# Kernel optimization log

Measured on AMD Instinct MI355X. Metric: run time of the kernel, lower is better.

## Reference

```python
import jax, jax.numpy as jnp
import numpy as np

WIN = 7  # window_size
NUM_HEADS = 8


def _relative_position_index(ws: int) -> np.ndarray:
    # Matches torch.meshgrid default ('ij') indexing used in the module.
    coords = np.stack(np.meshgrid(np.arange(ws), np.arange(ws), indexing='ij'))  # (2, ws, ws)
    flat = coords.reshape(2, -1)                                   # (2, ws*ws)
    rel = flat[:, :, None] - flat[:, None, :]                      # (2, N, N)
    rel = rel.transpose(1, 2, 0).copy()                            # (N, N, 2)
    rel[:, :, 0] += ws - 1
    rel[:, :, 1] += ws - 1
    rel[:, :, 0] *= 2 * ws - 1
    return rel.sum(-1)                                             # (N, N) int


def setup_inputs() -> dict:
    key = jax.random.key(0)
    ks = jax.random.split(key, 7)
    B_, N, C = 4096, WIN * WIN, 256
    nW = 64
    return {
        'x': jax.random.normal(ks[0], (B_, N, C), dtype=jnp.float32),
        'mask': jax.random.normal(ks[1], (nW, N, N), dtype=jnp.float32),
        'qkv_w': jax.random.normal(ks[2], (3 * C, C), dtype=jnp.float32) * 0.02,
        'qkv_b': jax.random.normal(ks[3], (3 * C,), dtype=jnp.float32) * 0.02,
        'proj_w': jax.random.normal(ks[4], (C, C), dtype=jnp.float32) * 0.02,
        'proj_b': jax.random.normal(ks[5], (C,), dtype=jnp.float32) * 0.02,
        'rpb_table': jax.random.normal(ks[6], ((2 * WIN - 1) ** 2, NUM_HEADS), dtype=jnp.float32) * 0.02,
    }


def reference(x, mask, qkv_w, qkv_b, proj_w, proj_b, rpb_table):
    B_, N, C = x.shape
    H = NUM_HEADS
    hd = C // H
    scale = hd ** -0.5
    rpi = jnp.asarray(_relative_position_index(WIN))  # (N, N) int, constant

    qkv = x @ qkv_w.T + qkv_b                          # (B_, N, 3C)
    qkv = qkv.reshape(B_, N, 3, H, hd).transpose(2, 0, 3, 1, 4)  # (3, B_, H, N, hd)
    q, k, v = qkv[0], qkv[1], qkv[2]

    attn = jnp.einsum('bhnd,bhmd->bhnm', q * scale, k)  # (B_, H, N, N)
    bias = rpb_table[rpi.reshape(-1)].reshape(N, N, H).transpose(2, 0, 1)  # (H, N, N)
    attn = attn + bias[None]

    nW = mask.shape[0]
    attn = attn.reshape(B_ // nW, nW, H, N, N) + mask[None, :, None]
    attn = attn.reshape(B_, H, N, N)
    attn = jax.nn.softmax(attn, axis=-1)

    out = jnp.einsum('bhnm,bhmd->bhnd', attn, v)       # (B_, H, N, hd)
    out = out.transpose(0, 2, 1, 3).reshape(B_, N, C)
    return out @ proj_w.T + proj_b
```

## Files before the change

### kernel.cpp

```cpp
#include <hip/hip_runtime.h>

#define SEG 51380224

typedef __attribute__((ext_vector_type(8))) __bf16 bf16x8;
typedef __attribute__((ext_vector_type(4))) __bf16 bf16x4;
typedef __attribute__((ext_vector_type(4))) float f32x4;

static __device__ __forceinline__ bf16x8 bzero8() {
    bf16x8 z;
#pragma unroll
    for (int u = 0; u < 8; ++u) z[u] = (__bf16)0.0f;
    return z;
}

static __device__ __forceinline__ void gl_lds16(const __bf16* g, __bf16* l) {
    __builtin_amdgcn_global_load_lds(
        (const __attribute__((address_space(1))) void*)g,
        (__attribute__((address_space(3))) void*)l, 16, 0, 0);
}

__global__ __launch_bounds__(256)
void cvt_bf16_k(const float* __restrict__ src, __bf16* __restrict__ dst, int n8)
{
    int i = blockIdx.x * 256 + threadIdx.x;
    const int stride = gridDim.x * 256;
    for (; i < n8; i += stride) {
        float4 a = *reinterpret_cast<const float4*>(src + (size_t)i * 8);
        float4 b = *reinterpret_cast<const float4*>(src + (size_t)i * 8 + 4);
        bf16x8 o;
        o[0] = (__bf16)a.x; o[1] = (__bf16)a.y; o[2] = (__bf16)a.z; o[3] = (__bf16)a.w;
        o[4] = (__bf16)b.x; o[5] = (__bf16)b.y; o[6] = (__bf16)b.z; o[7] = (__bf16)b.w;
        *reinterpret_cast<bf16x8*>(dst + (size_t)i * 8) = o;
    }
}

__global__ __launch_bounds__(256)
void expand_add_k(const float* __restrict__ mask, const float* __restrict__ rpb,
                  float* __restrict__ add)
{
    const int wh = blockIdx.x;
    const int w = wh >> 3, h = wh & 7;
    for (int e = threadIdx.x; e < 4096; e += 256) {
        int i = e >> 6, j = e & 63;
        float v = -1e30f;
        if (i < 49 && j < 49) {
            int ih = i / 7, iw = i - ih * 7;
            int jh = j / 7, jw = j - jh * 7;
            int bidx = (ih - jh + 6) * 13 + (iw - jw + 6);
            v = mask[(size_t)w * 2401 + i * 49 + j] + rpb[bidx * 8 + h];
        }
        add[(size_t)wh * 4096 + e] = v;
    }
}

__global__ __launch_bounds__(256)
void qkv_gemm_k(const __bf16* __restrict__ x, const __bf16* __restrict__ w,
                const float* __restrict__ bvec, __bf16* __restrict__ ws)
{
    __shared__ __bf16 As[2][128][64];
    __shared__ __bf16 Bs[2][128][64];
    const int tid  = threadIdx.x;
    const int nwg  = 1568 * 6;
    const int bid  = blockIdx.x;
    const int v    = (bid & 7) * (nwg >> 3) + (bid >> 3);
    const int mb   = v / 6, nb = v - mb * 6;
    const int m0   = mb * 128;
    const int n0   = nb * 128;
    const int wave = tid >> 6, lane = tid & 63;
    const int wm   = wave >> 1, wn = wave & 1;
    const int quad = lane >> 4, lm = lane & 15;

    const int srow = wave * 8 + (lane >> 3);
    const int scol = (((lane & 7) ^ (lane >> 3)) << 3);

    f32x4 acc[4][4] = {};

#pragma unroll
    for (int i = 0; i < 4; ++i) {
        int row = i * 32 + srow;
        gl_lds16(x + (size_t)(m0 + row) * 256 + 0 + scol,
                 &As[0][0][0] + i * 2048 + wave * 512);
        gl_lds16(w + (size_t)(n0 + row) * 256 + 0 + scol,
                 &Bs[0][0][0] + i * 2048 + wave * 512);
    }
    asm volatile("s_waitcnt vmcnt(0)" ::: "memory");
    __builtin_amdgcn_s_barrier();

#pragma unroll
    for (int t = 0; t < 4; ++t) {
        if (t < 3) {
            const int k0 = (t + 1) * 64;
            const int nb2 = (t + 1) & 1;
#pragma unroll
            for (int i = 0; i < 4; ++i) {
                int row = i * 32 + srow;
                gl_lds16(x + (size_t)(m0 + row) * 256 + k0 + scol,
                         &As[nb2][0][0] + i * 2048 + wave * 512);
                gl_lds16(w + (size_t)(n0 + row) * 256 + k0 + scol,
                         &Bs[nb2][0][0] + i * 2048 + wave * 512);
            }
        }
        const __bf16* Ab = &As[t & 1][0][0];
        const __bf16* Bb = &Bs[t & 1][0][0];
        __builtin_amdgcn_s_setprio(1);
#pragma unroll
        for (int kk = 0; kk < 64; kk += 32) {
            const int cl = (kk >> 3) + quad;
            bf16x8 af[4], bfr[4];
#pragma unroll
            for (int mt = 0; mt < 4; ++mt) {
                int row = wm * 64 + mt * 16 + lm;
                af[mt] = *reinterpret_cast<const bf16x8*>(Ab + row * 64 + ((cl ^ (lm & 7)) << 3));
            }
#pragma unroll
            for (int nt = 0; nt < 4; ++nt) {
                int row = wn * 64 + nt * 16 + lm;
                bfr[nt] = *reinterpret_cast<const bf16x8*>(Bb + row * 64 + ((cl ^ (lm & 7)) << 3));
            }
#pragma unroll
            for (int mt = 0; mt < 4; ++mt)
#pragma unroll
                for (int nt = 0; nt < 4; ++nt)
                    acc[mt][nt] = __builtin_amdgcn_mfma_f32_16x16x32_bf16(af[mt], bfr[nt], acc[mt][nt], 0, 0, 0);
        }
        __builtin_amdgcn_s_setprio(0);
        asm volatile("s_waitcnt vmcnt(0)" ::: "memory");
        __builtin_amdgcn_s_barrier();
    }

    const int   c3   = n0 >> 8;
    const float scl  = (c3 == 0) ? 0.17677669529663687f : 1.0f;
    __bf16*     segp = ws + (size_t)c3 * SEG;
    const int   n0c  = n0 & 255;
    char*       Cs   = (char*)&As[0][0][0];

#pragma unroll
    for (int nt = 0; nt < 4; ++nt) {
        float bj = bvec[n0 + wn * 64 + nt * 16 + lm];
#pragma unroll
        for (int mt = 0; mt < 4; ++mt)
#pragma unroll
            for (int r = 0; r < 4; ++r) {
                int row = wm * 64 + mt * 16 + quad * 4 + r;
                int byteoff = (row << 8) + ((wn * 64 + nt * 16 + lm) << 1);
                byteoff ^= (row & 0xC) << 2;
                *reinterpret_cast<__bf16*>(Cs + byteoff) =
                    (__bf16)((acc[mt][nt][r] + bj) * scl);
            }
    }
    __syncthreads();
#pragma unroll
    for (int it = 0; it < 8; ++it) {
        int row = it * 16 + (tid >> 4);
        int byteoff = (row << 8) + ((tid & 15) << 4);
        byteoff ^= (row & 0xC) << 2;
        bf16x8 c8 = *reinterpret_cast<const bf16x8*>(Cs + byteoff);
        *reinterpret_cast<bf16x8*>(segp + (size_t)(m0 + row) * 256 + n0c + ((tid & 15) << 3)) = c8;
    }
}

__global__ __launch_bounds__(64)
void attn_mfma_k(const __bf16* __restrict__ ws, const float* __restrict__ add,
                 __bf16* __restrict__ pre)
{
    __shared__ __bf16 Pl[64 * 72];
    __shared__ __bf16 Vt[32 * 72];
    const int lane = threadIdx.x;
    const int bh   = blockIdx.x;
    const int b    = bh >> 3, h = bh & 7;
    const int wh   = ((b & 63) << 3) | h;
    const int quad = lane >> 4, lm = lane & 15;
    const int koff = quad * 8;

    const __bf16* qp = ws + (size_t)(b * 49) * 256 + h * 32;
    const __bf16* kp = qp + SEG;
    const __bf16* vp = qp + (size_t)2 * SEG;

    {
        int d = lane >> 1, j0 = 48 + (lane & 1) * 8;
        *reinterpret_cast<bf16x8*>(&Vt[d * 72 + j0]) = bzero8();
    }
#pragma unroll
    for (int t = 0; t < 4; ++t) {
        int idx = lane + t * 64;
        if (idx < 196) {
            int j = idx >> 2, c8 = (idx & 3) * 8;
            bf16x8 vv = *reinterpret_cast<const bf16x8*>(vp + j * 256 + c8);
#pragma unroll
            for (int u = 0; u < 8; ++u) Vt[(c8 + u) * 72 + j] = vv[u];
        }
    }

    bf16x8 qf[4], kf[4];
#pragma unroll
    for (int t = 0; t < 4; ++t)
        qf[t] = *reinterpret_cast<const bf16x8*>(qp + (t * 16 + lm) * 256 + koff);
#pragma unroll
    for (int t = 0; t < 4; ++t) {
        int m = t * 16 + lm;
        kf[t] = (m < 49) ? *reinterpret_cast<const bf16x8*>(kp + m * 256 + koff)
                         : bzero8();
    }

    f32x4 s[4][4] = {};
#pragma unroll
    for (int mt = 0; mt < 4; ++mt)
#pragma unroll
        for (int nt = 0; nt < 4; ++nt)
            s[mt][nt] = __builtin_amdgcn_mfma_f32_16x16x32_bf16(kf[mt], qf[nt], s[mt][nt], 0, 0, 0);

    const float* ap = add + (size_t)wh * 4096;
#pragma unroll
    for (int nt = 0; nt < 4; ++nt) {
        int i = nt * 16 + lm;
#pragma unroll
        for (int mt = 0; mt < 4; ++mt) {
            f32x4 a4 = *reinterpret_cast<const f32x4*>(ap + i * 64 + mt * 16 + quad * 4);
            s[mt][nt] += a4;
        }
    }

#pragma unroll
    for (int nt = 0; nt < 4; ++nt) {
        float mx = -3.0e38f;
#pragma unroll
        for (int mt = 0; mt < 4; ++mt)
#pragma unroll
            for (int r = 0; r < 4; ++r) mx = fmaxf(mx, s[mt][nt][r]);
        mx = fmaxf(mx, __shfl_xor(mx, 16));
        mx = fmaxf(mx, __shfl_xor(mx, 32));
        float sum = 0.f;
#pragma unroll
        for (int mt = 0; mt < 4; ++mt)
#pragma unroll
            for (int r = 0; r < 4; ++r) {
                float e = __expf(s[mt][nt][r] - mx);
                s[mt][nt][r] = e; sum += e;
            }
        sum += __shfl_xor(sum, 16);
        sum += __shfl_xor(sum, 32);
        float rl = 1.0f / sum;
#pragma unroll
        for (int mt = 0; mt < 4; ++mt)
#pragma unroll
            for (int r = 0; r < 4; ++r) s[mt][nt][r] *= rl;
    }

#pragma unroll
    for (int nt = 0; nt < 4; ++nt) {
        int i = nt * 16 + lm;
#pragma unroll
        for (int mt = 0; mt < 4; ++mt) {
            bf16x4 p4;
#pragma unroll
            for (int r = 0; r < 4; ++r) p4[r] = (__bf16)s[mt][nt][r];
            *reinterpret_cast<bf16x4*>(&Pl[i * 72 + mt * 16 + quad * 4]) = p4;
        }
    }
    __syncthreads();

    f32x4 o[4][2] = {};
#pragma unroll
    for (int kt = 0; kt < 2; ++kt) {
        bf16x8 vf[2];
#pragma unroll
        for (int dt = 0; dt < 2; ++dt)
            vf[dt] = *reinterpret_cast<const bf16x8*>(&Vt[(dt * 16 + lm) * 72 + kt * 32 + koff]);
#pragma unroll
        for (int mt2 = 0; mt2 < 4; ++mt2) {
            bf16x8 pf = *reinterpret_cast<const bf16x8*>(&Pl[(mt2 * 16 + lm) * 72 + kt * 32 + koff]);
#pragma unroll
            for (int dt = 0; dt < 2; ++dt)
                o[mt2][dt] = __builtin_amdgcn_mfma_f32_16x16x32_bf16(pf, vf[dt], o[mt2][dt], 0, 0, 0);
        }
    }

    __syncthreads();
    __bf16* Ol = &Vt[0];
#pragma unroll
    for (int mt2 = 0; mt2 < 4; ++mt2)
#pragma unroll
        for (int dt = 0; dt < 2; ++dt)
#pragma unroll
            for (int r = 0; r < 4; ++r)
                Ol[(mt2 * 16 + quad * 4 + r) * 32 + dt * 16 + lm] = (__bf16)o[mt2][dt][r];
    __syncthreads();
#pragma unroll
    for (int it = 0; it < 4; ++it) {
        int i = it * 16 + (lane >> 2);
        if (i < 49) {
            bf16x8 v8 = *reinterpret_cast<const bf16x8*>(&Ol[i * 32 + (lane & 3) * 8]);
            *reinterpret_cast<bf16x8*>(pre + ((size_t)(b * 49 + i)) * 256 + h * 32 + (lane & 3) * 8) = v8;
        }
    }
}

__global__ __launch_bounds__(256)
void proj_gemm_k(const __bf16* __restrict__ pre, const __bf16* __restrict__ w,
                 const float* __restrict__ bvec, float* __restrict__ out)
{
    __shared__ __bf16 As[2][128][64];
    __shared__ __bf16 Bs[2][128][64];
    const int tid  = threadIdx.x;
    const int nwg  = 1568 * 2;
    const int bid  = blockIdx.x;
    const int v    = (bid & 7) * (nwg >> 3) + (bid >> 3);
    const int mb   = v >> 1, nb = v & 1;
    const int m0   = mb * 128;
    const int n0   = nb * 128;
    const int wave = tid >> 6, lane = tid & 63;
    const int wm   = wave >> 1, wn = wave & 1;
    const int quad = lane >> 4, lm = lane & 15;

    const int srow = wave * 8 + (lane >> 3);
    const int scol = (((lane & 7) ^ (lane >> 3)) << 3);

    f32x4 acc[4][4] = {};

#pragma unroll
    for (int i = 0; i < 4; ++i) {
        int row = i * 32 + srow;
        gl_lds16(pre + (size_t)(m0 + row) * 256 + 0 + scol,
                 &As[0][0][0] + i * 2048 + wave * 512);
        gl_lds16(w + (size_t)(n0 + row) * 256 + 0 + scol,
                 &Bs[0][0][0] + i * 2048 + wave * 512);
    }
    asm volatile("s_waitcnt vmcnt(0)" ::: "memory");
    __builtin_amdgcn_s_barrier();

#pragma unroll
    for (int t = 0; t < 4; ++t) {
        if (t < 3) {
            const int k0 = (t + 1) * 64;
            const int nb2 = (t + 1) & 1;
#pragma unroll
            for (int i = 0; i < 4; ++i) {
                int row = i * 32 + srow;
                gl_lds16(pre + (size_t)(m0 + row) * 256 + k0 + scol,
                         &As[nb2][0][0] + i * 2048 + wave * 512);
                gl_lds16(w + (size_t)(n0 + row) * 256 + k0 + scol,
                         &Bs[nb2][0][0] + i * 2048 + wave * 512);
            }
        }
        const __bf16* Ab = &As[t & 1][0][0];
        const __bf16* Bb = &Bs[t & 1][0][0];
        __builtin_amdgcn_s_setprio(1);
#pragma unroll
        for (int kk = 0; kk < 64; kk += 32) {
            const int cl = (kk >> 3) + quad;
            bf16x8 af[4], bfr[4];
#pragma unroll
            for (int mt = 0; mt < 4; ++mt) {
                int row = wm * 64 + mt * 16 + lm;
                af[mt] = *reinterpret_cast<const bf16x8*>(Ab + row * 64 + ((cl ^ (lm & 7)) << 3));
            }
#pragma unroll
            for (int nt = 0; nt < 4; ++nt) {
                int row = wn * 64 + nt * 16 + lm;
                bfr[nt] = *reinterpret_cast<const bf16x8*>(Bb + row * 64 + ((cl ^ (lm & 7)) << 3));
            }
#pragma unroll
            for (int mt = 0; mt < 4; ++mt)
#pragma unroll
                for (int nt = 0; nt < 4; ++nt)
                    acc[mt][nt] = __builtin_amdgcn_mfma_f32_16x16x32_bf16(af[mt], bfr[nt], acc[mt][nt], 0, 0, 0);
        }
        __builtin_amdgcn_s_setprio(0);
        asm volatile("s_waitcnt vmcnt(0)" ::: "memory");
        __builtin_amdgcn_s_barrier();
    }

#pragma unroll
    for (int nt = 0; nt < 4; ++nt) {
        int j = n0 + wn*64 + nt*16 + lm;
        float bj = bvec[j];
#pragma unroll
        for (int mt = 0; mt < 4; ++mt)
#pragma unroll
            for (int r = 0; r < 4; ++r) {
                int m = m0 + wm*64 + mt*16 + quad*4 + r;
                out[(size_t)m*256 + j] = acc[mt][nt][r] + bj;
            }
    }
}

extern "C" void kernel_launch(void* const* d_in, const int* in_sizes, int n_in,
                              void* d_out, int out_size, void* d_ws, size_t ws_size,
                              hipStream_t stream)
{
    const float* x      = (const float*)d_in[0];
    const float* mask   = (const float*)d_in[1];
    const float* qkv_w  = (const float*)d_in[2];
    const float* qkv_b  = (const float*)d_in[3];
    const float* proj_w = (const float*)d_in[4];
    const float* proj_b = (const float*)d_in[5];
    const float* rpb    = (const float*)d_in[6];

    __bf16* ws  = (__bf16*)d_ws;
    __bf16* pre = ws + (size_t)3 * SEG;
    float*  out = (float*)d_out;

    char*   ob      = (char*)d_out;
    float*  addbuf  = (float*)ob;
    __bf16* qkv_wb  = (__bf16*)(ob + (10u << 20));
    __bf16* xb      = (__bf16*)(ob + (16u << 20));
    __bf16* proj_wb = ws;

    cvt_bf16_k<<<dim3(2048), 256, 0, stream>>>(x, xb, 51380224 / 8);
    cvt_bf16_k<<<dim3(96),   256, 0, stream>>>(qkv_w, qkv_wb, 196608 / 8);
    expand_add_k<<<dim3(512), 256, 0, stream>>>(mask, rpb, addbuf);
    qkv_gemm_k<<<dim3(1568 * 6), 256, 0, stream>>>(xb, qkv_wb, qkv_b, ws);
    attn_mfma_k<<<dim3(32768), 64, 0, stream>>>(ws, addbuf, pre);
    cvt_bf16_k<<<dim3(32),   256, 0, stream>>>(proj_w, proj_wb, 65536 / 8);
    proj_gemm_k<<<dim3(1568 * 2), 256, 0, stream>>>(pre, proj_wb, proj_b, out);
}
```

Baseline: 781.6 us.

## Fuse prep kernels, shrink GEMM K-tile to 32, use nontemporal stores

Merges the x and qkv_w bf16 conversions and the mask+bias expansion into one prep kernel, removing two launches. Both GEMMs now use a K-step of 32 with half the LDS (32 KB), a matching swizzle and 8 pipeline stages, which may allow higher occupancy but adds barriers per tile. Output stores in the QKV and projection GEMMs become nontemporal to avoid polluting cache.

```diff
diff --git a/kernel.cpp b/kernel.cpp
--- a/kernel.cpp
+++ b/kernel.cpp
@@ -19,46 +19,71 @@
         (__attribute__((address_space(3))) void*)l, 16, 0, 0);
 }
 
+static __device__ __forceinline__ void cvt8(const float* src, __bf16* dst, int i) {
+    float4 a = *reinterpret_cast<const float4*>(src + (size_t)i * 8);
+    float4 b = *reinterpret_cast<const float4*>(src + (size_t)i * 8 + 4);
+    bf16x8 o;
+    o[0] = (__bf16)a.x; o[1] = (__bf16)a.y; o[2] = (__bf16)a.z; o[3] = (__bf16)a.w;
+    o[4] = (__bf16)b.x; o[5] = (__bf16)b.y; o[6] = (__bf16)b.z; o[7] = (__bf16)b.w;
+    *reinterpret_cast<bf16x8*>(dst + (size_t)i * 8) = o;
+}
+
+__global__ __launch_bounds__(256)
+void prep_k(const float* __restrict__ x, __bf16* __restrict__ xb,
+            const float* __restrict__ qw, __bf16* __restrict__ qwb,
+            const float* __restrict__ mask, const float* __restrict__ rpb,
+            float* __restrict__ add)
+{
+    const int NX = 51380224 / 8;
+    const int NW = 196608 / 8;
+    const int NE = 2097152 / 8;
+    int idx = blockIdx.x * 256 + threadIdx.x;
+    const int stride = gridDim.x * 256;
+    for (; idx < NX + NW + NE; idx += stride) {
+        if (idx < NX) {
+            cvt8(x, xb, idx);
+        } else if (idx < NX + NW) {
+            cvt8(qw, qwb, idx - NX);
+        } else {
+            int e = (idx - NX - NW) * 8;
+            int wh = e >> 12, within = e & 4095;
+            int i = within >> 6, j0 = within & 63;
+            int w = wh >> 3, h = wh & 7;
+            int ih = i / 7, iw = i - ih * 7;
+            float o[8];
+#pragma unroll
+            for (int u = 0; u < 8; ++u) {
+                int j = j0 + u;
+                float v = -1e30f;
+                if (i < 49 && j < 49) {
+                    int jh = j / 7, jw = j - jh * 7;
+                    int bidx = (ih - jh + 6) * 13 + (iw - jw + 6);
+                    v = mask[(size_t)w * 2401 + i * 49 + j] + rpb[bidx * 8 + h];
+                }
+                o[u] = v;
+            }
+            float* dst = add + (size_t)wh * 4096 + i * 64 + j0;
+            *reinterpret_cast<f32x4*>(dst)     = f32x4{o[0], o[1], o[2], o[3]};
+            *reinterpret_cast<f32x4*>(dst + 4) = f32x4{o[4], o[5], o[6], o[7]};
+        }
+    }
+}
+
 __global__ __launch_bounds__(256)
 void cvt_bf16_k(const float* __restrict__ src, __bf16* __restrict__ dst, int n8)
 {
     int i = blockIdx.x * 256 + threadIdx.x;
     const int stride = gridDim.x * 256;
-    for (; i < n8; i += stride) {
-        float4 a = *reinterpret_cast<const float4*>(src + (size_t)i * 8);
-        float4 b = *reinterpret_cast<const float4*>(src + (size_t)i * 8 + 4);
-        bf16x8 o;
-        o[0] = (__bf16)a.x; o[1] = (__bf16)a.y; o[2] = (__bf16)a.z; o[3] = (__bf16)a.w;
-        o[4] = (__bf16)b.x; o[5] = (__bf16)b.y; o[6] = (__bf16)b.z; o[7] = (__bf16)b.w;
-        *reinterpret_cast<bf16x8*>(dst + (size_t)i * 8) = o;
-    }
-}
-
-__global__ __launch_bounds__(256)
-void expand_add_k(const float* __restrict__ mask, const float* __restrict__ rpb,
-                  float* __restrict__ add)
-{
-    const int wh = blockIdx.x;
-    const int w = wh >> 3, h = wh & 7;
-    for (int e = threadIdx.x; e < 4096; e += 256) {
-        int i = e >> 6, j = e & 63;
-        float v = -1e30f;
-        if (i < 49 && j < 49) {
-            int ih = i / 7, iw = i - ih * 7;
-            int jh = j / 7, jw = j - jh * 7;
-            int bidx = (ih - jh + 6) * 13 + (iw - jw + 6);
-            v = mask[(size_t)w * 2401 + i * 49 + j] + rpb[bidx * 8 + h];
-        }
-        add[(size_t)wh * 4096 + e] = v;
-    }
+    for (; i < n8; i += stride) cvt8(src, dst, i);
 }
 
 __global__ __launch_bounds__(256)
 void qkv_gemm_k(const __bf16* __restrict__ x, const __bf16* __restrict__ w,
                 const float* __restrict__ bvec, __bf16* __restrict__ ws)
 {
-    __shared__ __bf16 As[2][128][64];
-    __shared__ __bf16 Bs[2][128][64];
+    __shared__ __attribute__((aligned(16))) char smem[32768];
+    __bf16* Asm = (__bf16*)smem;
+    __bf16* Bsm = (__bf16*)(smem + 16384);
     const int tid  = threadIdx.x;
     const int nwg  = 1568 * 6;
     const int bid  = blockIdx.x;
@@ -70,59 +95,53 @@
     const int wm   = wave >> 1, wn = wave & 1;
     const int quad = lane >> 4, lm = lane & 15;
 
-    const int srow = wave * 8 + (lane >> 3);
-    const int scol = (((lane & 7) ^ (lane >> 3)) << 3);
+    const int srow = wave * 16 + (lane >> 2);
+    const int scol = (((lane & 3) ^ ((lane >> 2) & 3)) << 3);
 
     f32x4 acc[4][4] = {};
 
 #pragma unroll
-    for (int i = 0; i < 4; ++i) {
-        int row = i * 32 + srow;
-        gl_lds16(x + (size_t)(m0 + row) * 256 + 0 + scol,
-                 &As[0][0][0] + i * 2048 + wave * 512);
-        gl_lds16(w + (size_t)(n0 + row) * 256 + 0 + scol,
-                 &Bs[0][0][0] + i * 2048 + wave * 512);
+    for (int i = 0; i < 2; ++i) {
+        gl_lds16(x + (size_t)(m0 + i * 64 + srow) * 256 + 0 + scol,
+                 Asm + i * 2048 + wave * 512);
+        gl_lds16(w + (size_t)(n0 + i * 64 + srow) * 256 + 0 + scol,
+                 Bsm + i * 2048 + wave * 512);
     }
     asm volatile("s_waitcnt vmcnt(0)" ::: "memory");
     __builtin_amdgcn_s_barrier();
 
 #pragma unroll
-    for (int t = 0; t < 4; ++t) {
-        if (t < 3) {
-            const int k0 = (t + 1) * 64;
-            const int nb2 = (t + 1) & 1;
-#pragma unroll
-            for (int i = 0; i < 4; ++i) {
-                int row = i * 32 + srow;
-                gl_lds16(x + (size_t)(m0 + row) * 256 + k0 + scol,
-                         &As[nb2][0][0] + i * 2048 + wave * 512);
-                gl_lds16(w + (size_t)(n0 + row) * 256 + k0 + scol,
-                         &Bs[nb2][0][0] + i * 2048 + wave * 512);
-            }
-        }
-        const __bf16* Ab = &As[t & 1][0][0];
-        const __bf16* Bb = &Bs[t & 1][0][0];
+    for (int t = 0; t < 8; ++t) {
+        const int cur = t & 1, nxt = cur ^ 1;
+        if (t < 7) {
+            const int k0 = (t + 1) * 32;
+#pragma unroll
+            for (int i = 0; i < 2; ++i) {
+                gl_lds16(x + (size_t)(m0 + i * 64 + srow) * 256 + k0 + scol,
+                         Asm + nxt * 4096 + i * 2048 + wave * 512);
+                gl_lds16(w + (size_t)(n0 + i * 64 + srow) * 256 + k0 + scol,
+                         Bsm + nxt * 4096 + i * 2048 + wave * 512);
+            }
+        }
+        const __bf16* Ab = Asm + cur * 4096;
+        const __bf16* Bb = Bsm + cur * 4096;
         __builtin_amdgcn_s_setprio(1);
-#pragma unroll
-        for (int kk = 0; kk < 64; kk += 32) {
-            const int cl = (kk >> 3) + quad;
-            bf16x8 af[4], bfr[4];
-#pragma unroll
-            for (int mt = 0; mt < 4; ++mt) {
-                int row = wm * 64 + mt * 16 + lm;
-                af[mt] = *reinterpret_cast<const bf16x8*>(Ab + row * 64 + ((cl ^ (lm & 7)) << 3));
-            }
-#pragma unroll
-            for (int nt = 0; nt < 4; ++nt) {
-                int row = wn * 64 + nt * 16 + lm;
-                bfr[nt] = *reinterpret_cast<const bf16x8*>(Bb + row * 64 + ((cl ^ (lm & 7)) << 3));
-            }
-#pragma unroll
-            for (int mt = 0; mt < 4; ++mt)
-#pragma unroll
-                for (int nt = 0; nt < 4; ++nt)
-                    acc[mt][nt] = __builtin_amdgcn_mfma_f32_16x16x32_bf16(af[mt], bfr[nt], acc[mt][nt], 0, 0, 0);
-        }
+        bf16x8 af[4], bfr[4];
+#pragma unroll
+        for (int mt = 0; mt < 4; ++mt) {
+            int row = wm * 64 + mt * 16 + lm;
+            af[mt] = *reinterpret_cast<const bf16x8*>(Ab + row * 32 + ((quad ^ (lm & 3)) << 3));
+        }
+#pragma unroll
+        for (int nt = 0; nt < 4; ++nt) {
+            int row = wn * 64 + nt * 16 + lm;
+            bfr[nt] = *reinterpret_cast<const bf16x8*>(Bb + row * 32 + ((quad ^ (lm & 3)) << 3));
+        }
+#pragma unroll
+        for (int mt = 0; mt < 4; ++mt)
+#pragma unroll
+            for (int nt = 0; nt < 4; ++nt)
+                acc[mt][nt] = __builtin_amdgcn_mfma_f32_16x16x32_bf16(af[mt], bfr[nt], acc[mt][nt], 0, 0, 0);
         __builtin_amdgcn_s_setprio(0);
         asm volatile("s_waitcnt vmcnt(0)" ::: "memory");
         __builtin_amdgcn_s_barrier();
@@ -132,7 +151,7 @@
     const float scl  = (c3 == 0) ? 0.17677669529663687f : 1.0f;
     __bf16*     segp = ws + (size_t)c3 * SEG;
     const int   n0c  = n0 & 255;
-    char*       Cs   = (char*)&As[0][0][0];
+    char*       Cs   = smem;
 
 #pragma unroll
     for (int nt = 0; nt < 4; ++nt) {
@@ -155,7 +174,8 @@
         int byteoff = (row << 8) + ((tid & 15) << 4);
         byteoff ^= (row & 0xC) << 2;
         bf16x8 c8 = *reinterpret_cast<const bf16x8*>(Cs + byteoff);
-        *reinterpret_cast<bf16x8*>(segp + (size_t)(m0 + row) * 256 + n0c + ((tid & 15) << 3)) = c8;
+        __builtin_nontemporal_store(c8,
+            reinterpret_cast<bf16x8*>(segp + (size_t)(m0 + row) * 256 + n0c + ((tid & 15) << 3)));
     }
 }
 
@@ -299,8 +319,9 @@
 void proj_gemm_k(const __bf16* __restrict__ pre, const __bf16* __restrict__ w,
                  const float* __restrict__ bvec, float* __restrict__ out)
 {
-    __shared__ __bf16 As[2][128][64];
-    __shared__ __bf16 Bs[2][128][64];
+    __shared__ __attribute__((aligned(16))) char smem[32768];
+    __bf16* Asm = (__bf16*)smem;
+    __bf16* Bsm = (__bf16*)(smem + 16384);
     const int tid  = threadIdx.x;
     const int nwg  = 1568 * 2;
     const int bid  = blockIdx.x;
@@ -312,59 +333,53 @@
     const int wm   = wave >> 1, wn = wave & 1;
     const int quad = lane >> 4, lm = lane & 15;
 
-    const int srow = wave * 8 + (lane >> 3);
-    const int scol = (((lane & 7) ^ (lane >> 3)) << 3);
+    const int srow = wave * 16 + (lane >> 2);
+    const int scol = (((lane & 3) ^ ((lane >> 2) & 3)) << 3);
 
     f32x4 acc[4][4] = {};
 
 #pragma unroll
-    for (int i = 0; i < 4; ++i) {
-        int row = i * 32 + srow;
-        gl_lds16(pre + (size_t)(m0 + row) * 256 + 0 + scol,
-                 &As[0][0][0] + i * 2048 + wave * 512);
-        gl_lds16(w + (size_t)(n0 + row) * 256 + 0 + scol,
-                 &Bs[0][0][0] + i * 2048 + wave * 512);
+    for (int i = 0; i < 2; ++i) {
+        gl_lds16(pre + (size_t)(m0 + i * 64 + srow) * 256 + 0 + scol,
+                 Asm + i * 2048 + wave * 512);
+        gl_lds16(w + (size_t)(n0 + i * 64 + srow) * 256 + 0 + scol,
+                 Bsm + i * 2048 + wave * 512);
     }
     asm volatile("s_waitcnt vmcnt(0)" ::: "memory");
     __builtin_amdgcn_s_barrier();
 
 #pragma unroll
-    for (int t = 0; t < 4; ++t) {
-        if (t < 3) {
-            const int k0 = (t + 1) * 64;
-            const int nb2 = (t + 1) & 1;
-#pragma unroll
-            for (int i = 0; i < 4; ++i) {
-                int row = i * 32 + srow;
-                gl_lds16(pre + (size_t)(m0 + row) * 256 + k0 + scol,
-                         &As[nb2][0][0] + i * 2048 + wave * 512);
-                gl_lds16(w + (size_t)(n0 + row) * 256 + k0 + scol,
-                         &Bs[nb2][0][0] + i * 2048 + wave * 512);
-            }
-        }
-        const __bf16* Ab = &As[t & 1][0][0];
-        const __bf16* Bb = &Bs[t & 1][0][0];
+    for (int t = 0; t < 8; ++t) {
+        const int cur = t & 1, nxt = cur ^ 1;
+        if (t < 7) {
+            const int k0 = (t + 1) * 32;
+#pragma unroll
+            for (int i = 0; i < 2; ++i) {
+                gl_lds16(pre + (size_t)(m0 + i * 64 + srow) * 256 + k0 + scol,
+                         Asm + nxt * 4096 + i * 2048 + wave * 512);
+                gl_lds16(w + (size_t)(n0 + i * 64 + srow) * 256 + k0 + scol,
+                         Bsm + nxt * 4096 + i * 2048 + wave * 512);
+            }
+        }
+        const __bf16* Ab = Asm + cur * 4096;
+        const __bf16* Bb = Bsm + cur * 4096;
         __builtin_amdgcn_s_setprio(1);
-#pragma unroll
-        for (int kk = 0; kk < 64; kk += 32) {
-            const int cl = (kk >> 3) + quad;
-            bf16x8 af[4], bfr[4];
-#pragma unroll
-            for (int mt = 0; mt < 4; ++mt) {
-                int row = wm * 64 + mt * 16 + lm;
-                af[mt] = *reinterpret_cast<const bf16x8*>(Ab + row * 64 + ((cl ^ (lm & 7)) << 3));
-            }
-#pragma unroll
-            for (int nt = 0; nt < 4; ++nt) {
-                int row = wn * 64 + nt * 16 + lm;
-                bfr[nt] = *reinterpret_cast<const bf16x8*>(Bb + row * 64 + ((cl ^ (lm & 7)) << 3));
-            }
-#pragma unroll
-            for (int mt = 0; mt < 4; ++mt)
-#pragma unroll
-                for (int nt = 0; nt < 4; ++nt)
-                    acc[mt][nt] = __builtin_amdgcn_mfma_f32_16x16x32_bf16(af[mt], bfr[nt], acc[mt][nt], 0, 0, 0);
-        }
+        bf16x8 af[4], bfr[4];
+#pragma unroll
+        for (int mt = 0; mt < 4; ++mt) {
+            int row = wm * 64 + mt * 16 + lm;
+            af[mt] = *reinterpret_cast<const bf16x8*>(Ab + row * 32 + ((quad ^ (lm & 3)) << 3));
+        }
+#pragma unroll
+        for (int nt = 0; nt < 4; ++nt) {
+            int row = wn * 64 + nt * 16 + lm;
+            bfr[nt] = *reinterpret_cast<const bf16x8*>(Bb + row * 32 + ((quad ^ (lm & 3)) << 3));
+        }
+#pragma unroll
+        for (int mt = 0; mt < 4; ++mt)
+#pragma unroll
+            for (int nt = 0; nt < 4; ++nt)
+                acc[mt][nt] = __builtin_amdgcn_mfma_f32_16x16x32_bf16(af[mt], bfr[nt], acc[mt][nt], 0, 0, 0);
         __builtin_amdgcn_s_setprio(0);
         asm volatile("s_waitcnt vmcnt(0)" ::: "memory");
         __builtin_amdgcn_s_barrier();
@@ -379,7 +394,7 @@
 #pragma unroll
             for (int r = 0; r < 4; ++r) {
                 int m = m0 + wm*64 + mt*16 + quad*4 + r;
-                out[(size_t)m*256 + j] = acc[mt][nt][r] + bj;
+                __builtin_nontemporal_store(acc[mt][nt][r] + bj, &out[(size_t)m*256 + j]);
             }
     }
 }
@@ -406,9 +421,7 @@
     __bf16* xb      = (__bf16*)(ob + (16u << 20));
     __bf16* proj_wb = ws;
 
-    cvt_bf16_k<<<dim3(2048), 256, 0, stream>>>(x, xb, 51380224 / 8);
-    cvt_bf16_k<<<dim3(96),   256, 0, stream>>>(qkv_w, qkv_wb, 196608 / 8);
-    expand_add_k<<<dim3(512), 256, 0, stream>>>(mask, rpb, addbuf);
+    prep_k<<<dim3(2048), 256, 0, stream>>>(x, xb, qkv_w, qkv_wb, mask, rpb, addbuf);
     qkv_gemm_k<<<dim3(1568 * 6), 256, 0, stream>>>(xb, qkv_wb, qkv_b, ws);
     attn_mfma_k<<<dim3(32768), 64, 0, stream>>>(ws, addbuf, pre);
     cvt_bf16_k<<<dim3(32),   256, 0, stream>>>(proj_w, proj_wb, 65536 / 8);
```

Result: faster. 741.7 us (-5.1%).
